# Optimization experiments

Measured on AMD Instinct MI355X. Metric: run time of the kernel, lower is better.

## Reference

```python
import jax, jax.numpy as jnp
import numpy as np

D = 512  # common_dim

def _ln(x, g, b):
    m = jnp.mean(x, -1, keepdims=True)
    v = jnp.var(x, -1, keepdims=True)
    return g * (x - m) * jax.lax.rsqrt(v + 1e-5) + b

def _gelu(x):
    return jax.nn.gelu(x, approximate=False)  # torch nn.GELU default (erf)

def _mha(q, kv, Wi, bi, Wo, bo):
    # seq_len == 1: softmax over a single key is exactly 1 regardless of q/k,
    # so MultiheadAttention reduces to out_proj(v_proj(kv)); identical math,
    # and q/k projections receive exactly zero gradient either way.
    vp = kv @ Wi[:, 2 * D:] + bi[2 * D:]
    return vp @ Wo + bo

def setup_inputs() -> dict:
    key = jax.random.key(0)
    ks = iter(jax.random.split(key, 64))
    B, HID = 8192, 1024
    Fv, Fi, Ft = 10, 6, 15
    def rn(shape, s=0.02):
        return jax.random.normal(next(ks), shape, jnp.float32) * s
    return dict(
        verb_hidden=rn((B, HID), 1.0), verb_logits=rn((B, Fv), 1.0),
        inst_hidden=rn((B, HID), 1.0), inst_logits=rn((B, Fi), 1.0),
        target_hidden=rn((B, HID), 1.0), target_logits=rn((B, Ft), 1.0),
        # hidden_projection per task (order: verb, instrument, target)
        hp_W=rn((3, HID, D)), hp_b=jnp.zeros((3, D)), hp_g=jnp.ones((3, D)), hp_be=jnp.zeros((3, D)),
        # logit_projection per task (different in-dims)
        lp_W_verb=rn((Fv, D // 2)), lp_b_verb=jnp.zeros((D // 2,)),
        lp_W_inst=rn((Fi, D // 2)), lp_b_inst=jnp.zeros((D // 2,)),
        lp_W_target=rn((Ft, D // 2)), lp_b_target=jnp.zeros((D // 2,)),
        lp_g=jnp.ones((3, D // 2)), lp_be=jnp.zeros((3, D // 2)),
        # 4 MHA modules: [self, verb_inst, verb_target, inst_target]
        mha_in_W=rn((4, D, 3 * D)), mha_in_b=jnp.zeros((4, 3 * D)),
        mha_out_W=rn((4, D, D)), mha_out_b=jnp.zeros((4, D)),
        n1_g=jnp.ones((3, D)), n1_be=jnp.zeros((3, D)),
        n2_g=jnp.ones((3, D)), n2_be=jnp.zeros((3, D)),
        gate_W=rn((3, 2 * D, D)), gate_b=jnp.zeros((3, D)),
        fus_W1=rn((3 * D + 3 * (D // 2), D)), fus_b1=jnp.zeros((D,)),
        fus_g1=jnp.ones((D,)), fus_ge1=jnp.zeros((D,)),
        fus_W2=rn((D, D)), fus_b2=jnp.zeros((D,)),
        fus_g2=jnp.ones((D,)), fus_ge2=jnp.zeros((D,)),
    )

def reference(verb_hidden, verb_logits, inst_hidden, inst_logits, target_hidden, target_logits,
              hp_W, hp_b, hp_g, hp_be,
              lp_W_verb, lp_b_verb, lp_W_inst, lp_b_inst, lp_W_target, lp_b_target, lp_g, lp_be,
              mha_in_W, mha_in_b, mha_out_W, mha_out_b,
              n1_g, n1_be, n2_g, n2_be, gate_W, gate_b,
              fus_W1, fus_b1, fus_g1, fus_ge1, fus_W2, fus_b2, fus_g2, fus_ge2):
    # dropout is inference-mode identity
    def hproj(x, i):
        return _gelu(_ln(x @ hp_W[i] + hp_b[i], hp_g[i], hp_be[i]))
    def lproj(x, W, b, i):
        return _gelu(_ln(jax.nn.sigmoid(x) @ W + b, lp_g[i], lp_be[i]))

    verb_h, inst_h, target_h = hproj(verb_hidden, 0), hproj(inst_hidden, 1), hproj(target_hidden, 2)
    verb_l = lproj(verb_logits, lp_W_verb, lp_b_verb, 0)
    inst_l = lproj(inst_logits, lp_W_inst, lp_b_inst, 1)
    target_l = lproj(target_logits, lp_W_target, lp_b_target, 2)

    sa = lambda x: _mha(x, x, mha_in_W[0], mha_in_b[0], mha_out_W[0], mha_out_b[0])
    verb_e = _ln(verb_h + sa(verb_h), n1_g[0], n1_be[0])
    inst_e = _ln(inst_h + sa(inst_h), n1_g[1], n1_be[1])
    target_e = _ln(target_h + sa(target_h), n1_g[2], n1_be[2])

    ca = lambda i, q, kv: _mha(q, kv, mha_in_W[i], mha_in_b[i], mha_out_W[i], mha_out_b[i])
    v2i, i2v = ca(1, verb_e, inst_e), ca(1, inst_e, verb_e)
    v2t, t2v = ca(2, verb_e, target_e), ca(2, target_e, verb_e)
    i2t, t2i = ca(3, inst_e, target_e), ca(3, target_e, inst_e)

    def fuse(x, a, b, i):
        m = (a + b) * 0.5
        gate = jax.nn.sigmoid(jnp.concatenate([x, m], axis=1) @ gate_W[i] + gate_b[i])
        return _ln(x + gate * m, n2_g[i], n2_be[i])

    verb_f = fuse(verb_e, v2i, v2t, 0)
    inst_f = fuse(inst_e, i2v, i2t, 1)
    target_f = fuse(target_e, t2v, t2i, 2)

    comb = jnp.concatenate([verb_f, inst_f, target_f, verb_l, inst_l, target_l], axis=1)  # [B, 2304]
    h = _gelu(_ln(comb @ fus_W1 + fus_b1, fus_g1, fus_ge1))
    return _ln(h @ fus_W2 + fus_b2, fus_g2, fus_ge2)
```

## Files before the change

### kernel.cpp

```cpp
#include <hip/hip_runtime.h>
#include <math.h>

typedef unsigned short ushort_t;
using short8  = __attribute__((ext_vector_type(8))) short;
using floatx4 = __attribute__((ext_vector_type(4))) float;

__device__ __forceinline__ ushort_t f2bf(float f) {
  unsigned u = __builtin_bit_cast(unsigned, f);
  u = (u + 0x7fffu + ((u >> 16) & 1u)) >> 16;
  return (ushort_t)u;
}
__device__ __forceinline__ float bf2f(ushort_t u) {
  unsigned v = ((unsigned)u) << 16;
  return __builtin_bit_cast(float, v);
}

__device__ __forceinline__ void load_lds16(const ushort_t* g, ushort_t* l) {
  __builtin_amdgcn_global_load_lds(
      (const __attribute__((address_space(1))) unsigned int*)g,
      (__attribute__((address_space(3))) unsigned int*)l, 16, 0, 0);
}

struct Seg { const ushort_t* A; const ushort_t* W; int lda, ldw, K; };
struct GemmZ {
  ushort_t* Cb;
  ushort_t* CbT;
  const float* bias;
  float scale; int nseg; int mmax;
  Seg seg[6];
};
struct GemmArgs { GemmZ z[9]; };

template <int BM>
__device__ __forceinline__ void gemm_body(const GemmArgs& ga) {
  const GemmZ& gz = ga.z[blockIdx.z];
  if ((int)blockIdx.x >= gz.mmax) return;
  __shared__ ushort_t As[BM * 64];
  __shared__ ushort_t Bs[128 * 64];
  const int tid = threadIdx.x;
  const int wid = tid >> 6, lane = tid & 63, quad = lane >> 4, l16 = lane & 15;
  const int bm = blockIdx.x * BM, bn = blockIdx.y * 128;
  constexpr int MI = BM / 32;
  const int wm = (wid & 1) * (BM / 2), wn = (wid >> 1) * 64;
  floatx4 acc[MI][4] = {};
  const int srow = tid >> 3;
  const int scol = ((tid & 7) ^ (srow & 7)) << 3;
  const int x7 = l16 & 7;

  for (int s = 0; s < gz.nseg; s++) {
    const Seg sg = gz.seg[s];
    const ushort_t* aG = sg.A + (size_t)(bm + srow) * sg.lda + scol;
    const ushort_t* bG = sg.W + (size_t)(bn + srow) * sg.ldw + scol;
    for (int k0 = 0; k0 < sg.K; k0 += 64) {
      __syncthreads();
#pragma unroll
      for (int r = 0; r < BM / 32; r++)
        load_lds16(aG + k0 + (size_t)(32 * r) * sg.lda, As + r * 2048 + tid * 8);
#pragma unroll
      for (int r = 0; r < 4; r++)
        load_lds16(bG + k0 + (size_t)(32 * r) * sg.ldw, Bs + r * 2048 + tid * 8);
      __syncthreads();
      short8 bw[4][2];
#pragma unroll
      for (int j = 0; j < 4; j++)
#pragma unroll
        for (int h = 0; h < 2; h++)
          bw[j][h] = *(const short8*)&Bs[(wn + 16 * j + l16) * 64 + (((quad + 4 * h) ^ x7) << 3)];
#pragma unroll
      for (int i = 0; i < MI; i++) {
        const int rb = (wm + 16 * i + l16) * 64;
        short8 a0 = *(const short8*)&As[rb + ((quad ^ x7) << 3)];
        short8 a1 = *(const short8*)&As[rb + (((quad + 4) ^ x7) << 3)];
#pragma unroll
        for (int j = 0; j < 4; j++) {
          acc[i][j] = __builtin_amdgcn_mfma_f32_16x16x32_bf16(a0, bw[j][0], acc[i][j], 0, 0, 0);
          acc[i][j] = __builtin_amdgcn_mfma_f32_16x16x32_bf16(a1, bw[j][1], acc[i][j], 0, 0, 0);
        }
      }
    }
  }

#pragma unroll
  for (int i = 0; i < MI; i++) {
#pragma unroll
    for (int j = 0; j < 4; j++) {
      const int colg = bn + wn + 16 * j + l16;
      const float bb = gz.bias ? gz.bias[colg] : 0.f;
#pragma unroll
      for (int r = 0; r < 4; r++) {
        const int rowg = bm + wm + 16 * i + quad * 4 + r;
        const float v = (acc[i][j][r] + bb) * gz.scale;
        const ushort_t bo = f2bf(v);
        if (gz.Cb)  gz.Cb[(size_t)rowg * 512 + colg] = bo;
        if (gz.CbT) gz.CbT[(size_t)colg * 512 + rowg] = bo;
      }
    }
  }
}

__global__ __launch_bounds__(256) void gemm_L2(GemmArgs ga)  { gemm_body<128>(ga); }
__global__ __launch_bounds__(256) void gemm_L4(GemmArgs ga)  { gemm_body<128>(ga); }
__global__ __launch_bounds__(256) void gemm_L7(GemmArgs ga)  { gemm_body<128>(ga); }
__global__ __launch_bounds__(256) void gemm_L9(GemmArgs ga)  { gemm_body<128>(ga); }
__global__ __launch_bounds__(256) void gemm_L11(GemmArgs ga) { gemm_body<64>(ga); }
__global__ __launch_bounds__(256) void gemm_L13(GemmArgs ga) { gemm_body<64>(ga); }

__global__ __launch_bounds__(256) void row_ln(
    const ushort_t* __restrict__ P, const ushort_t* __restrict__ R,
    const ushort_t* __restrict__ cross,
    const float* __restrict__ gamma, const float* __restrict__ beta, int gstride,
    ushort_t* __restrict__ outb, float* __restrict__ outf, int mode, int gelu)
{
  const size_t S2 = (size_t)8192 * 512;
  const int wid = threadIdx.x >> 6, lane = threadIdx.x & 63;
  const int row = blockIdx.x * 4 + wid;
  const int t = row >> 13;
  const float* g  = gamma + t * gstride;
  const float* be = beta + t * gstride;
  const ushort_t* p = P + (size_t)row * 512;
  const ushort_t* ar = nullptr;
  if (mode == 2) ar = cross + (size_t)t * S2 + (size_t)(row & 8191) * 512;
  float v[8], s = 0.f, ss = 0.f;
#pragma unroll
  for (int j = 0; j < 8; j++) {
    const int c = lane + j * 64;
    float x = bf2f(p[c]);
    if (mode == 2) {
      const float sg = 1.f / (1.f + __expf(-x));
      x = bf2f(R[(size_t)row * 512 + c]) + sg * bf2f(ar[c]);
    } else if (mode == 1) {
      x += bf2f(R[(size_t)row * 512 + c]);
    }
    v[j] = x; s += x; ss += x * x;
  }
#pragma unroll
  for (int off = 32; off > 0; off >>= 1) {
    s  += __shfl_xor(s,  off, 64);
    ss += __shfl_xor(ss, off, 64);
  }
  const float mean = s * (1.f / 512.f);
  const float var  = ss * (1.f / 512.f) - mean * mean;
  const float rstd = rsqrtf(var + 1e-5f);
#pragma unroll
  for (int j = 0; j < 8; j++) {
    const int c = lane + j * 64;
    float y = g[c] * ((v[j] - mean) * rstd) + be[c];
    if (gelu) y = 0.5f * y * (1.f + erff(y * 0.70710678118f));
    if (outb) outb[(size_t)row * 512 + c] = f2bf(y);
    else      outf[(size_t)row * 512 + c] = y;
  }
}

__global__ __launch_bounds__(256) void lproj3(
    const float* __restrict__ vl, const float* __restrict__ il, const float* __restrict__ tl,
    const float* __restrict__ Wv, const float* __restrict__ bv,
    const float* __restrict__ Wi, const float* __restrict__ bi,
    const float* __restrict__ Wt, const float* __restrict__ bt,
    const float* __restrict__ lp_g, const float* __restrict__ lp_be,
    ushort_t* __restrict__ out)
{
  const int set = blockIdx.y;
  const float* logits = set == 0 ? vl : set == 1 ? il : tl;
  const int F = set == 0 ? 10 : set == 1 ? 6 : 15;
  const float* W    = set == 0 ? Wv : set == 1 ? Wi : Wt;
  const float* bias = set == 0 ? bv : set == 1 ? bi : bt;
  const float* gamma = lp_g + set * 256;
  const float* beta  = lp_be + set * 256;
  ushort_t* o = out + (size_t)set * 8192 * 256;
  const int wid = threadIdx.x >> 6, lane = threadIdx.x & 63;
  const int row = blockIdx.x * 4 + wid;
  float sg[16];
  for (int f = 0; f < F; f++)
    sg[f] = 1.f / (1.f + __expf(-logits[(size_t)row * F + f]));
  float v[4], s = 0.f, ss = 0.f;
#pragma unroll
  for (int j = 0; j < 4; j++) {
    const int c = lane + j * 64;
    float a = bias[c];
    for (int f = 0; f < F; f++) a += sg[f] * W[f * 256 + c];
    v[j] = a; s += a; ss += a * a;
  }
#pragma unroll
  for (int off = 32; off > 0; off >>= 1) {
    s  += __shfl_xor(s,  off, 64);
    ss += __shfl_xor(ss, off, 64);
  }
  const float mean = s * (1.f / 256.f);
  const float var  = ss * (1.f / 256.f) - mean * mean;
  const float rstd = rsqrtf(var + 1e-5f);
#pragma unroll
  for (int j = 0; j < 4; j++) {
    const int c = lane + j * 64;
    float y = gamma[c] * ((v[j] - mean) * rstd) + beta[c];
    y = 0.5f * y * (1.f + erff(y * 0.70710678118f));
    o[(size_t)row * 256 + c] = f2bf(y);
  }
}

struct PrepArgs {
  const float *vh, *ih, *th;
  const float *mha_in_W, *mha_out_W, *mha_in_b, *mha_out_b;
  const float *hp_W, *gate_W, *fus_W1, *fus_W2;
  ushort_t *xbf, *Wvbf, *hpWt, *gateWt, *fusW1t, *fusW2t, *WoT;
  float *cb;
};

__global__ __launch_bounds__(256) void prep(PrepArgs pa) {
  __shared__ float tsh[32][33];
  const int b = blockIdx.x, tid = threadIdx.x;
  if (b < 24576) {
    const int mat = b >> 13, blk = b & 8191;
    const float* src = mat == 0 ? pa.vh : mat == 1 ? pa.ih : pa.th;
    const size_t i = (size_t)blk * 256 + tid;
    const float4 f = ((const float4*)src)[i];
    ushort4 o; o.x = f2bf(f.x); o.y = f2bf(f.y); o.z = f2bf(f.z); o.w = f2bf(f.w);
    ((ushort4*)(pa.xbf + (size_t)mat * 8192 * 1024))[i] = o;
    return;
  }
  if (b < 28672) {
    const int u = b - 24576, z = u >> 10, blk = u & 1023;
    const int idx = blk * 256 + tid, r = idx >> 9, c = idx & 511;
    pa.Wvbf[(size_t)z * 262144 + idx] =
        f2bf(pa.mha_in_W[(size_t)z * 786432 + (size_t)r * 1536 + 1024 + c]);
    return;
  }
  if (b >= 34176) {
    const int u2 = b - 34176, z = u2 >> 1, part = u2 & 1;
    const int n = part * 256 + tid;
    const float* bv = pa.mha_in_b + z * 1536 + 1024;
    const float* Wo = pa.mha_out_W + (size_t)z * 262144;
    float a = pa.mha_out_b[z * 512 + n];
    for (int k = 0; k < 512; k++) a += bv[k] * Wo[(size_t)k * 512 + n];
    pa.cb[z * 512 + n] = a;
    return;
  }
  const float* tin; ushort_t* tout; int K, N, u; size_t izs, ozs;
  if (b < 30208)      { u = b - 28672; tin = pa.hp_W;      tout = pa.hpWt;   K = 1024; N = 512; izs = 524288; ozs = 524288; }
  else if (b < 31744) { u = b - 30208; tin = pa.gate_W;    tout = pa.gateWt; K = 1024; N = 512; izs = 524288; ozs = 524288; }
  else if (b < 32896) { u = b - 31744; tin = pa.fus_W1;    tout = pa.fusW1t; K = 2304; N = 512; izs = 0;      ozs = 0; }
  else if (b < 33152) { u = b - 32896; tin = pa.fus_W2;    tout = pa.fusW2t; K = 512;  N = 512; izs = 0;      ozs = 0; }
  else                { u = b - 33152; tin = pa.mha_out_W; tout = pa.WoT;    K = 512;  N = 512; izs = 262144; ozs = 262144; }
  const int nbx = N / 32, perz = nbx * (K / 32);
  const int z = u / perz, rem = u % perz, bx = rem % nbx, by = rem / nbx;
  tin += (size_t)z * izs; tout += (size_t)z * ozs;
  const int n0 = bx * 32, k0 = by * 32;
  const int tx = tid & 31, ty = tid >> 5;
#pragma unroll
  for (int r = 0; r < 32; r += 8)
    tsh[ty + r][tx] = tin[(size_t)(k0 + ty + r) * N + n0 + tx];
  __syncthreads();
#pragma unroll
  for (int r = 0; r < 32; r += 8)
    tout[(size_t)(n0 + ty + r) * K + k0 + tx] = f2bf(tsh[tx][ty + r]);
}

__global__ __launch_bounds__(256) void bias2_k(
    const float* __restrict__ cb, const float* __restrict__ gate_W,
    const float* __restrict__ gate_b, float* __restrict__ out,
    float* __restrict__ out2)
{
  const int t = blockIdx.z;
  const int m1[3] = {1, 1, 2}, m2[3] = {2, 3, 3};
  const float* c1 = cb + m1[t] * 512;
  const float* c2 = cb + m2[t] * 512;
  const float* W = gate_W + (size_t)t * 524288 + (size_t)512 * 512;
  const int n = blockIdx.x * 256 + threadIdx.x;
  float a = gate_b[t * 512 + n];
  for (int k = 0; k < 512; k++) a += 0.5f * (c1[k] + c2[k]) * W[(size_t)k * 512 + n];
  out[t * 512 + n] = a;
  out2[t * 512 + n] = c1[n] + c2[n];
}

extern "C" void kernel_launch(void* const* d_in, const int* in_sizes, int n_in,
                              void* d_out, int out_size, void* d_ws, size_t ws_size,
                              hipStream_t stream)
{
  const float* verb_hidden   = (const float*)d_in[0];
  const float* verb_logits   = (const float*)d_in[1];
  const float* inst_hidden   = (const float*)d_in[2];
  const float* inst_logits   = (const float*)d_in[3];
  const float* target_hidden = (const float*)d_in[4];
  const float* target_logits = (const float*)d_in[5];
  const float* hp_W  = (const float*)d_in[6];
  const float* hp_b  = (const float*)d_in[7];
  const float* hp_g  = (const float*)d_in[8];
  const float* hp_be = (const float*)d_in[9];
  const float* lp_W_verb   = (const float*)d_in[10];
  const float* lp_b_verb   = (const float*)d_in[11];
  const float* lp_W_inst   = (const float*)d_in[12];
  const float* lp_b_inst   = (const float*)d_in[13];
  const float* lp_W_target = (const float*)d_in[14];
  const float* lp_b_target = (const float*)d_in[15];
  const float* lp_g  = (const float*)d_in[16];
  const float* lp_be = (const float*)d_in[17];
  const float* mha_in_W  = (const float*)d_in[18];
  const float* mha_in_b  = (const float*)d_in[19];
  const float* mha_out_W = (const float*)d_in[20];
  const float* mha_out_b = (const float*)d_in[21];
  const float* n1_g  = (const float*)d_in[22];
  const float* n1_be = (const float*)d_in[23];
  const float* n2_g  = (const float*)d_in[24];
  const float* n2_be = (const float*)d_in[25];
  const float* gate_W = (const float*)d_in[26];
  const float* gate_b = (const float*)d_in[27];
  const float* fus_W1 = (const float*)d_in[28];
  const float* fus_b1 = (const float*)d_in[29];
  const float* fus_g1 = (const float*)d_in[30];
  const float* fus_ge1= (const float*)d_in[31];
  const float* fus_W2 = (const float*)d_in[32];
  const float* fus_b2 = (const float*)d_in[33];
  const float* fus_g2 = (const float*)d_in[34];
  const float* fus_ge2= (const float*)d_in[35];

  char* w = (char*)d_ws;
  const size_t S2 = (size_t)8192 * 512;
  const size_t MB = 1024 * 1024;
  ushort_t* xbf     = (ushort_t*)(w);
  ushort_t* crossbf = (ushort_t*)(w);
  ushort_t* gbf     = (ushort_t*)(w);
  ushort_t* Pbig    = (ushort_t*)(w + 48 * MB);
  ushort_t* hbf     = (ushort_t*)(w + 72 * MB);
  ushort_t* fbf     = (ushort_t*)(w + 72 * MB);
  ushort_t* ebf     = (ushort_t*)(w + 96 * MB);
  ushort_t* lbf     = (ushort_t*)(w + 120 * MB);
  char* wp = w + 132 * MB;
  ushort_t* hpWt    = (ushort_t*)(wp);
  ushort_t* gateWt  = (ushort_t*)(wp + 3145728);
  ushort_t* fusW1t  = (ushort_t*)(wp + 6291456);
  ushort_t* fusW2t  = (ushort_t*)(wp + 8650752);
  ushort_t* WoT     = (ushort_t*)(wp + 9175040);
  ushort_t* Wvbf    = (ushort_t*)(wp + 11272192);
  ushort_t* CWt     = (ushort_t*)(wp + 13369344);
  ushort_t* CWplain = (ushort_t*)(wp + 15466496);
  ushort_t* Gt      = (ushort_t*)(wp + 17563648);
  float*    cb      = (float*)(wp + 20709376);
  float*    bias2   = (float*)(wp + 20717568);
  float*    cbsum   = (float*)(wp + 20723712);

  dim3 blk(256);
  const int mods[3][2] = {{1, 2}, {1, 3}, {2, 3}};
  const int srcs[3][2] = {{1, 2}, {0, 2}, {0, 1}};

  {
    PrepArgs pa;
    pa.vh = verb_hidden; pa.ih = inst_hidden; pa.th = target_hidden;
    pa.mha_in_W = mha_in_W; pa.mha_out_W = mha_out_W;
    pa.mha_in_b = mha_in_b; pa.mha_out_b = mha_out_b;
    pa.hp_W = hp_W; pa.gate_W = gate_W; pa.fus_W1 = fus_W1; pa.fus_W2 = fus_W2;
    pa.xbf = xbf; pa.Wvbf = Wvbf; pa.hpWt = hpWt; pa.gateWt = gateWt;
    pa.fusW1t = fusW1t; pa.fusW2t = fusW2t; pa.WoT = WoT; pa.cb = cb;
    prep<<<34184, blk, 0, stream>>>(pa);
  }

  {
    GemmArgs ga{};
    for (int z = 0; z < 4; z++) {
      GemmZ& g = ga.z[z];
      g.Cb = CWplain + (size_t)z * 262144; g.CbT = CWt + (size_t)z * 262144;
      g.scale = 1.f; g.nseg = 1; g.mmax = 4;
      g.seg[0] = {Wvbf + (size_t)z * 262144, WoT + (size_t)z * 262144, 512, 512, 512};
    }
    gemm_L2<<<dim3(4, 4, 4), blk, 0, stream>>>(ga);
  }

  bias2_k<<<dim3(2, 1, 3), blk, 0, stream>>>(cb, gate_W, gate_b, bias2, cbsum);

  {
    GemmArgs ga{};
    for (int z = 0; z < 3; z++) {
      GemmZ& g = ga.z[z];
      g.Cb = Pbig + (size_t)z * S2; g.bias = hp_b + z * 512;
      g.scale = 1.f; g.nseg = 1; g.mmax = 64;
      g.seg[0] = {xbf + (size_t)z * 8192 * 1024, hpWt + (size_t)z * 524288, 1024, 1024, 1024};
    }
    for (int idx = 0; idx < 6; idx++) {
      const int t = idx >> 1, u = idx & 1, m = mods[t][u];
      GemmZ& g = ga.z[3 + idx];
      g.Cb = Gt + (size_t)idx * 262144; g.scale = 0.5f; g.nseg = 1; g.mmax = 4;
      g.seg[0] = {gateWt + (size_t)t * 524288 + 512, CWplain + (size_t)m * 262144, 1024, 512, 512};
    }
    gemm_L4<<<dim3(64, 4, 9), blk, 0, stream>>>(ga);
  }

  lproj3<<<dim3(2048, 3), blk, 0, stream>>>(verb_logits, inst_logits, target_logits,
      lp_W_verb, lp_b_verb, lp_W_inst, lp_b_inst, lp_W_target, lp_b_target,
      lp_g, lp_be, lbf);

  row_ln<<<6144, blk, 0, stream>>>(Pbig, nullptr, nullptr, hp_g, hp_be, 512,
                                   hbf, nullptr, 0, 1);

  {
    GemmArgs ga{};
    GemmZ& g = ga.z[0];
    g.Cb = Pbig; g.bias = cb; g.scale = 1.f; g.nseg = 1; g.mmax = 192;
    g.seg[0] = {hbf, CWt, 512, 512, 512};
    gemm_L7<<<dim3(192, 4, 1), blk, 0, stream>>>(ga);
  }
  row_ln<<<6144, blk, 0, stream>>>(Pbig, hbf, nullptr, n1_g, n1_be, 512,
                                   ebf, nullptr, 1, 0);

  {
    GemmArgs ga{};
    for (int t = 0; t < 3; t++) {
      GemmZ& g = ga.z[t];
      g.Cb = crossbf + (size_t)t * S2;
      g.bias = cbsum + t * 512; g.scale = 0.5f; g.nseg = 2; g.mmax = 64;
      g.seg[0] = {ebf + (size_t)srcs[t][0] * S2, CWt + (size_t)mods[t][0] * 262144, 512, 512, 512};
      g.seg[1] = {ebf + (size_t)srcs[t][1] * S2, CWt + (size_t)mods[t][1] * 262144, 512, 512, 512};
    }
    for (int t = 0; t < 3; t++) {
      GemmZ& g = ga.z[3 + t];
      g.Cb = Pbig + (size_t)t * S2; g.bias = bias2 + t * 512;
      g.scale = 1.f; g.nseg = 3; g.mmax = 64;
      g.seg[0] = {ebf + (size_t)t * S2,           gateWt + (size_t)t * 524288, 512, 1024, 512};
      g.seg[1] = {ebf + (size_t)srcs[t][0] * S2,  Gt + (size_t)(2 * t) * 262144,     512, 512, 512};
      g.seg[2] = {ebf + (size_t)srcs[t][1] * S2,  Gt + (size_t)(2 * t + 1) * 262144, 512, 512, 512};
    }
    gemm_L9<<<dim3(64, 4, 6), blk, 0, stream>>>(ga);
  }

  row_ln<<<6144, blk, 0, stream>>>(Pbig, ebf, crossbf, n2_g, n2_be, 512,
                                   fbf, nullptr, 2, 0);

  {
    GemmArgs ga{};
    GemmZ& g = ga.z[0];
    g.Cb = Pbig; g.bias = fus_b1; g.scale = 1.f; g.nseg = 6; g.mmax = 128;
    g.seg[0] = {fbf,                          fusW1t,        512, 2304, 512};
    g.seg[1] = {fbf + S2,                     fusW1t + 512,  512, 2304, 512};
    g.seg[2] = {fbf + 2 * S2,                 fusW1t + 1024, 512, 2304, 512};
    g.seg[3] = {lbf,                          fusW1t + 1536, 256, 2304, 256};
    g.seg[4] = {lbf + (size_t)8192 * 256,     fusW1t + 1792, 256, 2304, 256};
    g.seg[5] = {lbf + (size_t)2 * 8192 * 256, fusW1t + 2048, 256, 2304, 256};
    gemm_L11<<<dim3(128, 4, 1), blk, 0, stream>>>(ga);
  }
  row_ln<<<2048, blk, 0, stream>>>(Pbig, nullptr, nullptr, fus_g1, fus_ge1, 0,
                                   gbf, nullptr, 0, 1);
  {
    GemmArgs ga{};
    GemmZ& g = ga.z[0];
    g.Cb = Pbig; g.bias = fus_b2; g.scale = 1.f; g.nseg = 1; g.mmax = 128;
    g.seg[0] = {gbf, fusW2t, 512, 512, 512};
    gemm_L13<<<dim3(128, 4, 1), blk, 0, stream>>>(ga);
  }
  row_ln<<<2048, blk, 0, stream>>>(Pbig, nullptr, nullptr, fus_g2, fus_ge2, 0,
                                   nullptr, (float*)d_out, 0, 0);
}
```

Before: 633.9 us.

## Double GEMM K-tile to 128 and split-K the small bias matvec kernels

The shared GEMM body now stages 128-wide K slices per iteration instead of 64, with a new 16-way XOR swizzle, halving the number of barrier pairs per K loop at the cost of twice the LDS per block (which may reduce occupancy). Separately, the bias-folding matvecs in prep and bias2_k are split across four K-quarters per output column with wave shuffles to reduce, launching four times as many blocks so these serial 512-long dot products have more parallelism.

Result: faster. 618.8 us (-2.4%).

```diff
diff --git a/kernel.cpp b/kernel.cpp
--- a/kernel.cpp
+++ b/kernel.cpp
@@ -35,46 +35,43 @@
 __device__ __forceinline__ void gemm_body(const GemmArgs& ga) {
   const GemmZ& gz = ga.z[blockIdx.z];
   if ((int)blockIdx.x >= gz.mmax) return;
-  __shared__ ushort_t As[BM * 64];
-  __shared__ ushort_t Bs[128 * 64];
+  __shared__ ushort_t As[BM * 128];
+  __shared__ ushort_t Bs[128 * 128];
   const int tid = threadIdx.x;
   const int wid = tid >> 6, lane = tid & 63, quad = lane >> 4, l16 = lane & 15;
   const int bm = blockIdx.x * BM, bn = blockIdx.y * 128;
   constexpr int MI = BM / 32;
   const int wm = (wid & 1) * (BM / 2), wn = (wid >> 1) * 64;
   floatx4 acc[MI][4] = {};
-  const int srow = tid >> 3;
-  const int scol = ((tid & 7) ^ (srow & 7)) << 3;
-  const int x7 = l16 & 7;
+  const int srow = tid >> 4;
+  const int scol = ((tid & 15) ^ srow) << 3;
 
   for (int s = 0; s < gz.nseg; s++) {
     const Seg sg = gz.seg[s];
     const ushort_t* aG = sg.A + (size_t)(bm + srow) * sg.lda + scol;
     const ushort_t* bG = sg.W + (size_t)(bn + srow) * sg.ldw + scol;
-    for (int k0 = 0; k0 < sg.K; k0 += 64) {
+    for (int k0 = 0; k0 < sg.K; k0 += 128) {
       __syncthreads();
 #pragma unroll
-      for (int r = 0; r < BM / 32; r++)
-        load_lds16(aG + k0 + (size_t)(32 * r) * sg.lda, As + r * 2048 + tid * 8);
-#pragma unroll
-      for (int r = 0; r < 4; r++)
-        load_lds16(bG + k0 + (size_t)(32 * r) * sg.ldw, Bs + r * 2048 + tid * 8);
+      for (int r = 0; r < BM / 16; r++)
+        load_lds16(aG + k0 + (size_t)(16 * r) * sg.lda, As + r * 2048 + tid * 8);
+#pragma unroll
+      for (int r = 0; r < 8; r++)
+        load_lds16(bG + k0 + (size_t)(16 * r) * sg.ldw, Bs + r * 2048 + tid * 8);
       __syncthreads();
-      short8 bw[4][2];
-#pragma unroll
-      for (int j = 0; j < 4; j++)
-#pragma unroll
-        for (int h = 0; h < 2; h++)
-          bw[j][h] = *(const short8*)&Bs[(wn + 16 * j + l16) * 64 + (((quad + 4 * h) ^ x7) << 3)];
-#pragma unroll
-      for (int i = 0; i < MI; i++) {
-        const int rb = (wm + 16 * i + l16) * 64;
-        short8 a0 = *(const short8*)&As[rb + ((quad ^ x7) << 3)];
-        short8 a1 = *(const short8*)&As[rb + (((quad + 4) ^ x7) << 3)];
-#pragma unroll
-        for (int j = 0; j < 4; j++) {
-          acc[i][j] = __builtin_amdgcn_mfma_f32_16x16x32_bf16(a0, bw[j][0], acc[i][j], 0, 0, 0);
-          acc[i][j] = __builtin_amdgcn_mfma_f32_16x16x32_bf16(a1, bw[j][1], acc[i][j], 0, 0, 0);
+#pragma unroll
+      for (int kw = 0; kw < 4; kw++) {
+        const int sl = ((kw * 4 + quad) ^ l16) << 3;
+        short8 bw[4];
+#pragma unroll
+        for (int j = 0; j < 4; j++)
+          bw[j] = *(const short8*)&Bs[(wn + 16 * j + l16) * 128 + sl];
+#pragma unroll
+        for (int i = 0; i < MI; i++) {
+          short8 af = *(const short8*)&As[(wm + 16 * i + l16) * 128 + sl];
+#pragma unroll
+          for (int j = 0; j < 4; j++)
+            acc[i][j] = __builtin_amdgcn_mfma_f32_16x16x32_bf16(af, bw[j], acc[i][j], 0, 0, 0);
         }
       }
     }
@@ -225,13 +222,22 @@
     return;
   }
   if (b >= 34176) {
-    const int u2 = b - 34176, z = u2 >> 1, part = u2 & 1;
-    const int n = part * 256 + tid;
+    const int u2 = b - 34176;
+    const int z = u2 >> 3, n0 = (u2 & 7) * 64;
+    const int lane = tid & 63, wv = tid >> 6;
+    const int o = lane & 15, p = lane >> 4;
+    const int n = n0 + wv * 16 + o;
     const float* bv = pa.mha_in_b + z * 1536 + 1024;
     const float* Wo = pa.mha_out_W + (size_t)z * 262144;
-    float a = pa.mha_out_b[z * 512 + n];
-    for (int k = 0; k < 512; k++) a += bv[k] * Wo[(size_t)k * 512 + n];
-    pa.cb[z * 512 + n] = a;
+    float a = 0.f;
+#pragma unroll 4
+    for (int kk = 0; kk < 128; kk++) {
+      const int k = p * 128 + kk;
+      a += bv[k] * Wo[(size_t)k * 512 + n];
+    }
+    a += __shfl_xor(a, 16, 64);
+    a += __shfl_xor(a, 32, 64);
+    if (p == 0) pa.cb[z * 512 + n] = a + pa.mha_out_b[z * 512 + n];
     return;
   }
   const float* tin; ushort_t* tout; int K, N, u; size_t izs, ozs;
@@ -264,11 +270,22 @@
   const float* c1 = cb + m1[t] * 512;
   const float* c2 = cb + m2[t] * 512;
   const float* W = gate_W + (size_t)t * 524288 + (size_t)512 * 512;
-  const int n = blockIdx.x * 256 + threadIdx.x;
-  float a = gate_b[t * 512 + n];
-  for (int k = 0; k < 512; k++) a += 0.5f * (c1[k] + c2[k]) * W[(size_t)k * 512 + n];
-  out[t * 512 + n] = a;
-  out2[t * 512 + n] = c1[n] + c2[n];
+  const int tid = threadIdx.x;
+  const int lane = tid & 63, wv = tid >> 6;
+  const int o = lane & 15, p = lane >> 4;
+  const int n = blockIdx.x * 64 + wv * 16 + o;
+  float a = 0.f;
+#pragma unroll 4
+  for (int kk = 0; kk < 128; kk++) {
+    const int k = p * 128 + kk;
+    a += 0.5f * (c1[k] + c2[k]) * W[(size_t)k * 512 + n];
+  }
+  a += __shfl_xor(a, 16, 64);
+  a += __shfl_xor(a, 32, 64);
+  if (p == 0) {
+    out[t * 512 + n] = a + gate_b[t * 512 + n];
+    out2[t * 512 + n] = c1[n] + c2[n];
+  }
 }
 
 extern "C" void kernel_launch(void* const* d_in, const int* in_sizes, int n_in,
@@ -349,7 +366,7 @@
     pa.hp_W = hp_W; pa.gate_W = gate_W; pa.fus_W1 = fus_W1; pa.fus_W2 = fus_W2;
     pa.xbf = xbf; pa.Wvbf = Wvbf; pa.hpWt = hpWt; pa.gateWt = gateWt;
     pa.fusW1t = fusW1t; pa.fusW2t = fusW2t; pa.WoT = WoT; pa.cb = cb;
-    prep<<<34184, blk, 0, stream>>>(pa);
+    prep<<<34208, blk, 0, stream>>>(pa);
   }
 
   {
@@ -363,7 +380,7 @@
     gemm_L2<<<dim3(4, 4, 4), blk, 0, stream>>>(ga);
   }
 
-  bias2_k<<<dim3(2, 1, 3), blk, 0, stream>>>(cb, gate_W, gate_b, bias2, cbsum);
+  bias2_k<<<dim3(8, 1, 3), blk, 0, stream>>>(cb, gate_W, gate_b, bias2, cbsum);
 
   {
     GemmArgs ga{};
```
